# Optimization experiments

Measured on AMD Instinct MI355X. Metric: run time of the kernel, lower is better.

The kernel has to match this reference:

```python
import jax, jax.numpy as jnp
import numpy as np

N = 50000
E = 800000
D_IN, D_HID, D_OUT = 128, 128, 64


def gcn_layer(x, src, dst, W, b, n_nodes):
    # GCNConv: h = W x; add self-loops; symmetric normalization deg^-1/2;
    # scatter-add messages from src to dst; add bias.
    h = x @ W  # [N, d_out]
    loop = jnp.arange(n_nodes, dtype=src.dtype)
    src_sl = jnp.concatenate([src, loop])  # [E+N]
    dst_sl = jnp.concatenate([dst, loop])
    deg = jax.ops.segment_sum(jnp.ones_like(dst_sl, dtype=h.dtype), dst_sl,
                              num_segments=n_nodes)  # in-degree incl. self-loop
    dis = jnp.where(deg > 0, jax.lax.rsqrt(deg), 0.0)
    norm = dis[src_sl] * dis[dst_sl]  # [E+N]
    msg = h[src_sl] * norm[:, None]  # gather + scale
    out = jax.ops.segment_sum(msg, dst_sl, num_segments=n_nodes)
    return out + b


def setup_inputs() -> dict:
    key = jax.random.key(0)
    ks = jax.random.split(key, 8)
    x = jax.random.normal(ks[0], (N, D_IN), dtype=jnp.float32)
    edge_index = jax.random.randint(ks[1], (2, E), 0, N, dtype=jnp.int32)
    def glorot(k, fan_in, fan_out):
        s = jnp.sqrt(6.0 / (fan_in + fan_out))
        return jax.random.uniform(k, (fan_in, fan_out), jnp.float32, -s, s)
    return {
        "x": x,
        "edge_index": edge_index,
        "W1": glorot(ks[2], D_IN, D_HID),  "b1": jnp.zeros((D_HID,), jnp.float32),
        "W2": glorot(ks[3], D_HID, D_HID), "b2": jnp.zeros((D_HID,), jnp.float32),
        "W3": glorot(ks[4], D_HID, D_OUT), "b3": jnp.zeros((D_OUT,), jnp.float32),
    }


def reference(x, edge_index, W1, b1, W2, b2, W3, b3):
    src, dst = edge_index[0], edge_index[1]
    n = x.shape[0]
    h = jax.nn.relu(gcn_layer(x, src, dst, W1, b1, n))
    h = jax.nn.relu(gcn_layer(h, src, dst, W2, b2, n))
    return gcn_layer(h, src, dst, W3, b3, n)
```

## Files before the change

kernel.cpp:

```cpp
#include <hip/hip_runtime.h>
#include <hip/hip_fp16.h>
#include <math.h>


typedef _Float16 half8 __attribute__((ext_vector_type(8)));
typedef float f32x4 __attribute__((ext_vector_type(4)));

__global__ void count_kernel(const int* __restrict__ dst, int* __restrict__ counts,
                             int* __restrict__ rank, int E) {
    int i = blockIdx.x * blockDim.x + threadIdx.x;
    int st = gridDim.x * blockDim.x;
    for (; i < E; i += st) rank[i] = atomicAdd(&counts[dst[i]], 1);
}

__global__ __launch_bounds__(256) void block_sum_kernel(const int* __restrict__ counts,
                                                        int* __restrict__ bsum, int n) {
    const int b = blockIdx.x;
    const int t = threadIdx.x;
    const int idx = b * 256 + t;
    int v = (idx < n) ? counts[idx] : 0;
#pragma unroll
    for (int o = 32; o > 0; o >>= 1) v += __shfl_down(v, o, 64);
    __shared__ int ws[4];
    if ((t & 63) == 0) ws[t >> 6] = v;
    __syncthreads();
    if (t == 0) bsum[b] = ws[0] + ws[1] + ws[2] + ws[3];
}

__global__ __launch_bounds__(256) void small_scan_kernel(int* __restrict__ bsum, int nb) {
    __shared__ int sm[256];
    const int t = threadIdx.x;
    int v = (t < nb) ? bsum[t] : 0;
    sm[t] = v;
    __syncthreads();
    for (int o = 1; o < 256; o <<= 1) {
        int x = (t >= o) ? sm[t - o] : 0;
        __syncthreads();
        sm[t] += x;
        __syncthreads();
    }
    if (t < nb) bsum[t] = sm[t] - v;
}

__global__ __launch_bounds__(256) void scan_block_kernel(const int* __restrict__ counts,
                                                         const int* __restrict__ bsum,
                                                         int* __restrict__ offs,
                                                         float* __restrict__ dis,
                                                         int n, int E) {
    const int b = blockIdx.x;
    const int t = threadIdx.x;
    const int idx = b * 256 + t;
    int v = (idx < n) ? counts[idx] : 0;
    if (idx < n) dis[idx] = rsqrtf((float)(v + 1));
    __shared__ int sm[256];
    sm[t] = v;
    __syncthreads();
    for (int o = 1; o < 256; o <<= 1) {
        int x = (t >= o) ? sm[t - o] : 0;
        __syncthreads();
        sm[t] += x;
        __syncthreads();
    }
    if (idx < n) offs[idx] = bsum[b] + sm[t] - v;
    if (idx == n) offs[n] = E;
}

__global__ void fill_kernel(const int* __restrict__ src, const int* __restrict__ dst,
                            const int* __restrict__ offs, const int* __restrict__ rank,
                            int* __restrict__ csr_s, int E) {
    int i = blockIdx.x * blockDim.x + threadIdx.x;
    int st = gridDim.x * blockDim.x;
    for (; i < E; i += st) {
        int p = offs[dst[i]] + rank[i];
        csr_s[p] = src[i];
    }
}

__global__ __launch_bounds__(256) void wsplit_kernel(const float* __restrict__ W1,
                                                     const float* __restrict__ W2,
                                                     const float* __restrict__ W3,
                                                     _Float16* __restrict__ hi,
                                                     _Float16* __restrict__ lo) {
    int idx = blockIdx.x * 256 + threadIdx.x;
    if (idx >= 40960) return;
    float v;
    if (idx < 16384) {
        int c = idx >> 7, k = idx & 127;
        v = W1[k * 128 + c];
    } else if (idx < 32768) {
        int j = idx - 16384;
        int c = j >> 7, k = j & 127;
        v = W2[k * 128 + c];
    } else {
        int j = idx - 32768;
        int c = j >> 7, k = j & 127;
        v = W3[k * 64 + c];
    }
    _Float16 h = (_Float16)v;
    hi[idx] = h;
    lo[idx] = (_Float16)(v - (float)h);
}

template <int NOUT, bool FROM_F32>
__device__ __forceinline__ void gemm_core(const half8* __restrict__ XhV,
                                          const _Float16* __restrict__ WThi,
                                          const _Float16* __restrict__ WTlo,
                                          const float* __restrict__ dis,
                                          _Float16* __restrict__ Y, int nrows,
                                          const float4* X4) {
    constexpr int CT = NOUT / 16;
    const int wave = threadIdx.x >> 6;
    const int lane = threadIdx.x & 63;
    const int lrow = lane & 15;
    const int lk = lane >> 4;
    const int r0 = (blockIdx.x * 4 + wave) * 32;

    const f32x4 Z = {0.f, 0.f, 0.f, 0.f};
    f32x4 acc[2][CT];
#pragma unroll
    for (int a = 0; a < 2; ++a)
#pragma unroll
        for (int b = 0; b < CT; ++b) acc[a][b] = Z;

    const half8* WhiV = (const half8*)WThi;
    const half8* WloV = (const half8*)WTlo;

    int ar0 = r0 + lrow;
    int ar1 = r0 + 16 + lrow;
    if (ar0 > nrows - 1) ar0 = nrows - 1;
    if (ar1 > nrows - 1) ar1 = nrows - 1;

#pragma unroll
    for (int ks = 0; ks < 4; ++ks) {
        const int kidx = ks * 4 + lk;
        half8 a0h, a1h, a0l, a1l;
        if constexpr (FROM_F32) {
            float4 u0 = X4[(size_t)ar0 * 32 + 2 * kidx];
            float4 u1 = X4[(size_t)ar0 * 32 + 2 * kidx + 1];
            float4 w0 = X4[(size_t)ar1 * 32 + 2 * kidx];
            float4 w1 = X4[(size_t)ar1 * 32 + 2 * kidx + 1];
            float v0[8] = {u0.x, u0.y, u0.z, u0.w, u1.x, u1.y, u1.z, u1.w};
            float v1[8] = {w0.x, w0.y, w0.z, w0.w, w1.x, w1.y, w1.z, w1.w};
#pragma unroll
            for (int j = 0; j < 8; ++j) {
                _Float16 hh = (_Float16)v0[j];
                a0h[j] = hh;
                a0l[j] = (_Float16)(v0[j] - (float)hh);
                _Float16 gg = (_Float16)v1[j];
                a1h[j] = gg;
                a1l[j] = (_Float16)(v1[j] - (float)gg);
            }
        } else {
            a0h = XhV[(size_t)ar0 * 16 + kidx];
            a1h = XhV[(size_t)ar1 * 16 + kidx];
        }
#pragma unroll
        for (int ct = 0; ct < CT; ++ct) {
            const size_t bidx = (size_t)(ct * 16 + lrow) * 16 + kidx;
            half8 bh = WhiV[bidx];
            half8 bl = WloV[bidx];
            if constexpr (FROM_F32) {
                acc[0][ct] = __builtin_amdgcn_mfma_f32_16x16x32_f16(a0l, bh, acc[0][ct], 0, 0, 0);
                acc[1][ct] = __builtin_amdgcn_mfma_f32_16x16x32_f16(a1l, bh, acc[1][ct], 0, 0, 0);
            }
            acc[0][ct] = __builtin_amdgcn_mfma_f32_16x16x32_f16(a0h, bl, acc[0][ct], 0, 0, 0);
            acc[0][ct] = __builtin_amdgcn_mfma_f32_16x16x32_f16(a0h, bh, acc[0][ct], 0, 0, 0);
            acc[1][ct] = __builtin_amdgcn_mfma_f32_16x16x32_f16(a1h, bl, acc[1][ct], 0, 0, 0);
            acc[1][ct] = __builtin_amdgcn_mfma_f32_16x16x32_f16(a1h, bh, acc[1][ct], 0, 0, 0);
        }
    }

    const int orow = r0 + lk * 4;
#pragma unroll
    for (int rt = 0; rt < 2; ++rt) {
#pragma unroll
        for (int r = 0; r < 4; ++r) {
            int row = orow + rt * 16 + r;
            if (row < nrows) {
                float dd = dis[row];
#pragma unroll
                for (int ct = 0; ct < CT; ++ct) {
                    Y[(size_t)row * NOUT + ct * 16 + lrow] =
                        (_Float16)(dd * acc[rt][ct][r]);
                }
            }
        }
    }
}

template <int NOUT>
__global__ __launch_bounds__(256) void gemm_mfma(const _Float16* __restrict__ Xh,
                                                 const _Float16* __restrict__ WThi,
                                                 const _Float16* __restrict__ WTlo,
                                                 const float* __restrict__ dis,
                                                 _Float16* __restrict__ Y, int nrows) {
    gemm_core<NOUT, false>((const half8*)Xh, WThi, WTlo, dis, Y, nrows, nullptr);
}

__global__ __launch_bounds__(256) void gemm_mfma_l1(const float* __restrict__ X,
                                                    const _Float16* __restrict__ WThi,
                                                    const _Float16* __restrict__ WTlo,
                                                    const float* __restrict__ dis,
                                                    _Float16* __restrict__ Y, int nrows) {
    gemm_core<128, true>(nullptr, WThi, WTlo, dis, Y, nrows, (const float4*)X);
}

#define ACC8(_v)                                                                    \
    do {                                                                            \
        float2 _f;                                                                  \
        _f = __half22float2(*reinterpret_cast<const __half2*>(&(_v).x));            \
        a0 += _f.x; a1 += _f.y;                                                     \
        _f = __half22float2(*reinterpret_cast<const __half2*>(&(_v).y));            \
        a2 += _f.x; a3 += _f.y;                                                     \
        _f = __half22float2(*reinterpret_cast<const __half2*>(&(_v).z));            \
        a4 += _f.x; a5 += _f.y;                                                     \
        _f = __half22float2(*reinterpret_cast<const __half2*>(&(_v).w));            \
        a6 += _f.x; a7 += _f.y;                                                     \
    } while (0)

#define ACC8W(_v, _scale)                                                           \
    do {                                                                            \
        float2 _f;                                                                  \
        _f = __half22float2(*reinterpret_cast<const __half2*>(&(_v).x));            \
        a0 = fmaf((_scale), _f.x, a0); a1 = fmaf((_scale), _f.y, a1);               \
        _f = __half22float2(*reinterpret_cast<const __half2*>(&(_v).y));            \
        a2 = fmaf((_scale), _f.x, a2); a3 = fmaf((_scale), _f.y, a3);               \
        _f = __half22float2(*reinterpret_cast<const __half2*>(&(_v).z));            \
        a4 = fmaf((_scale), _f.x, a4); a5 = fmaf((_scale), _f.y, a5);               \
        _f = __half22float2(*reinterpret_cast<const __half2*>(&(_v).w));            \
        a6 = fmaf((_scale), _f.x, a6); a7 = fmaf((_scale), _f.y, a7);               \
    } while (0)

template <bool RELU, bool F16OUT>
__global__ __launch_bounds__(256) void agg128_kernel(const __half* __restrict__ h,
                                                     const float* __restrict__ dis,
                                                     const int* __restrict__ offs,
                                                     const int* __restrict__ csr_s,
                                                     const float* __restrict__ bias,
                                                     float* __restrict__ outf,
                                                     __half* __restrict__ oh16, int n) {
    const int d = blockIdx.x * 4 + (threadIdx.x >> 6);
    if (d >= n) return;
    const int lane = threadIdx.x & 63;
    const int g = lane >> 4;
    const int p = lane & 15;
    const int beg = offs[d];
    const int end = offs[d + 1];
    const uint4* hv = (const uint4*)h;

    float a0 = 0.f, a1 = 0.f, a2 = 0.f, a3 = 0.f;
    float a4 = 0.f, a5 = 0.f, a6 = 0.f, a7 = 0.f;

    int i = beg;
    for (; i + 16 <= end; i += 16) {
        int r0 = csr_s[i + g];
        int r1 = csr_s[i + 4 + g];
        int r2 = csr_s[i + 8 + g];
        int r3 = csr_s[i + 12 + g];
        uint4 v0 = hv[(size_t)r0 * 16 + p];
        uint4 v1 = hv[(size_t)r1 * 16 + p];
        uint4 v2 = hv[(size_t)r2 * 16 + p];
        uint4 v3 = hv[(size_t)r3 * 16 + p];
        ACC8(v0); ACC8(v1); ACC8(v2); ACC8(v3);
    }
    if (i + 8 <= end) {
        int r0 = csr_s[i + g];
        int r1 = csr_s[i + 4 + g];
        uint4 v0 = hv[(size_t)r0 * 16 + p];
        uint4 v1 = hv[(size_t)r1 * 16 + p];
        ACC8(v0); ACC8(v1);
        i += 8;
    }
    if (i + 4 <= end) {
        int r0 = csr_s[i + g];
        uint4 v0 = hv[(size_t)r0 * 16 + p];
        ACC8(v0);
        i += 4;
    }
    {
        int m = end - i;
        int row = (g < m) ? csr_s[i + g] : d;
        float wt = (g <= m) ? 1.f : 0.f;
        uint4 v = hv[(size_t)row * 16 + p];
        ACC8W(v, wt);
    }

    a0 += __shfl_xor(a0, 16); a0 += __shfl_xor(a0, 32);
    a1 += __shfl_xor(a1, 16); a1 += __shfl_xor(a1, 32);
    a2 += __shfl_xor(a2, 16); a2 += __shfl_xor(a2, 32);
    a3 += __shfl_xor(a3, 16); a3 += __shfl_xor(a3, 32);
    a4 += __shfl_xor(a4, 16); a4 += __shfl_xor(a4, 32);
    a5 += __shfl_xor(a5, 16); a5 += __shfl_xor(a5, 32);
    a6 += __shfl_xor(a6, 16); a6 += __shfl_xor(a6, 32);
    a7 += __shfl_xor(a7, 16); a7 += __shfl_xor(a7, 32);

    if (lane < 16) {
        float dd = dis[d];
        float4 b0 = ((const float4*)bias)[2 * p];
        float4 b1 = ((const float4*)bias)[2 * p + 1];
        float r0 = fmaf(dd, a0, b0.x);
        float r1 = fmaf(dd, a1, b0.y);
        float r2 = fmaf(dd, a2, b0.z);
        float r3 = fmaf(dd, a3, b0.w);
        float r4 = fmaf(dd, a4, b1.x);
        float r5 = fmaf(dd, a5, b1.y);
        float r6 = fmaf(dd, a6, b1.z);
        float r7 = fmaf(dd, a7, b1.w);
        if (RELU) {
            r0 = fmaxf(r0, 0.f); r1 = fmaxf(r1, 0.f);
            r2 = fmaxf(r2, 0.f); r3 = fmaxf(r3, 0.f);
            r4 = fmaxf(r4, 0.f); r5 = fmaxf(r5, 0.f);
            r6 = fmaxf(r6, 0.f); r7 = fmaxf(r7, 0.f);
        }
        if constexpr (F16OUT) {
            __half2 q0 = __halves2half2(__float2half(r0), __float2half(r1));
            __half2 q1 = __halves2half2(__float2half(r2), __float2half(r3));
            __half2 q2 = __halves2half2(__float2half(r4), __float2half(r5));
            __half2 q3 = __halves2half2(__float2half(r6), __float2half(r7));
            uint4 uh;
            uh.x = *reinterpret_cast<unsigned*>(&q0);
            uh.y = *reinterpret_cast<unsigned*>(&q1);
            uh.z = *reinterpret_cast<unsigned*>(&q2);
            uh.w = *reinterpret_cast<unsigned*>(&q3);
            ((uint4*)oh16)[(size_t)d * 16 + p] = uh;
        } else {
            ((float4*)outf)[(size_t)d * 32 + 2 * p] = make_float4(r0, r1, r2, r3);
            ((float4*)outf)[(size_t)d * 32 + 2 * p + 1] = make_float4(r4, r5, r6, r7);
        }
    }
}

__global__ __launch_bounds__(256) void agg64_kernel(const __half* __restrict__ h,
                                                    const float* __restrict__ dis,
                                                    const int* __restrict__ offs,
                                                    const int* __restrict__ csr_s,
                                                    const float* __restrict__ bias,
                                                    float* __restrict__ outf, int n) {
    const int d = blockIdx.x * 4 + (threadIdx.x >> 6);
    if (d >= n) return;
    const int lane = threadIdx.x & 63;
    const int g = lane >> 3;
    const int p = lane & 7;
    const int beg = offs[d];
    const int end = offs[d + 1];
    const uint4* hv = (const uint4*)h;

    float a0 = 0.f, a1 = 0.f, a2 = 0.f, a3 = 0.f;
    float a4 = 0.f, a5 = 0.f, a6 = 0.f, a7 = 0.f;

    int i = beg;
    for (; i + 16 <= end; i += 16) {
        int r0 = csr_s[i + g];
        int r1 = csr_s[i + 8 + g];
        uint4 v0 = hv[(size_t)r0 * 8 + p];
        uint4 v1 = hv[(size_t)r1 * 8 + p];
        ACC8(v0); ACC8(v1);
    }
    if (i + 8 <= end) {
        int r0 = csr_s[i + g];
        uint4 v0 = hv[(size_t)r0 * 8 + p];
        ACC8(v0);
        i += 8;
    }
    {
        int m = end - i;
        int row = (g < m) ? csr_s[i + g] : d;
        float wt = (g <= m) ? 1.f : 0.f;
        uint4 v = hv[(size_t)row * 8 + p];
        ACC8W(v, wt);
    }

    a0 += __shfl_xor(a0, 8); a0 += __shfl_xor(a0, 16); a0 += __shfl_xor(a0, 32);
    a1 += __shfl_xor(a1, 8); a1 += __shfl_xor(a1, 16); a1 += __shfl_xor(a1, 32);
    a2 += __shfl_xor(a2, 8); a2 += __shfl_xor(a2, 16); a2 += __shfl_xor(a2, 32);
    a3 += __shfl_xor(a3, 8); a3 += __shfl_xor(a3, 16); a3 += __shfl_xor(a3, 32);
    a4 += __shfl_xor(a4, 8); a4 += __shfl_xor(a4, 16); a4 += __shfl_xor(a4, 32);
    a5 += __shfl_xor(a5, 8); a5 += __shfl_xor(a5, 16); a5 += __shfl_xor(a5, 32);
    a6 += __shfl_xor(a6, 8); a6 += __shfl_xor(a6, 16); a6 += __shfl_xor(a6, 32);
    a7 += __shfl_xor(a7, 8); a7 += __shfl_xor(a7, 16); a7 += __shfl_xor(a7, 32);

    if (lane < 8) {
        float dd = dis[d];
        float4 b0 = ((const float4*)bias)[2 * p];
        float4 b1 = ((const float4*)bias)[2 * p + 1];
        float r0 = fmaf(dd, a0, b0.x);
        float r1 = fmaf(dd, a1, b0.y);
        float r2 = fmaf(dd, a2, b0.z);
        float r3 = fmaf(dd, a3, b0.w);
        float r4 = fmaf(dd, a4, b1.x);
        float r5 = fmaf(dd, a5, b1.y);
        float r6 = fmaf(dd, a6, b1.z);
        float r7 = fmaf(dd, a7, b1.w);
        ((float4*)outf)[(size_t)d * 16 + 2 * p] = make_float4(r0, r1, r2, r3);
        ((float4*)outf)[(size_t)d * 16 + 2 * p + 1] = make_float4(r4, r5, r6, r7);
    }
}


extern "C" void kernel_launch(void* const* d_in, const int* in_sizes, int n_in,
                              void* d_out, int out_size, void* d_ws, size_t ws_size,
                              hipStream_t stream) {
    const float* x  = (const float*)d_in[0];
    const int*   ei = (const int*)d_in[1];
    const float* W1 = (const float*)d_in[2];
    const float* b1 = (const float*)d_in[3];
    const float* W2 = (const float*)d_in[4];
    const float* b2 = (const float*)d_in[5];
    const float* W3 = (const float*)d_in[6];
    const float* b3 = (const float*)d_in[7];

    const int N = in_sizes[0] / 128;
    const int E = in_sizes[1] / 2;
    const int* src = ei;
    const int* dst = ei + E;
    float* out = (float*)d_out;

    char* w = (char*)d_ws;
    auto take = [&](size_t bytes) -> void* {
        void* p = (void*)w;
        w += (bytes + 255) & ~(size_t)255;
        return p;
    };
    int*      counts = (int*)take((size_t)N * 4);
    int*      offs   = (int*)take((size_t)(N + 1) * 4);
    float*    dis    = (float*)take((size_t)N * 4);
    int*      bsum   = (int*)take((size_t)1024 * 4);
    int*      csr_s  = (int*)take((size_t)E * 4);
    _Float16* G16    = (_Float16*)take((size_t)N * 128 * 2);
    _Float16* H16    = (_Float16*)take((size_t)N * 128 * 2);
    _Float16* Whi    = (_Float16*)take((size_t)40960 * 2);
    _Float16* Wlo    = (_Float16*)take((size_t)40960 * 2);
    int*      rank   = (int*)G16;

    const int NBLK = (N + 256) / 256;

    hipMemsetAsync(counts, 0, (size_t)N * 4, stream);
    count_kernel<<<2048, 256, 0, stream>>>(dst, counts, rank, E);
    block_sum_kernel<<<NBLK, 256, 0, stream>>>(counts, bsum, N);
    small_scan_kernel<<<1, 256, 0, stream>>>(bsum, NBLK);
    scan_block_kernel<<<NBLK, 256, 0, stream>>>(counts, bsum, offs, dis, N, E);
    fill_kernel<<<2048, 256, 0, stream>>>(src, dst, offs, rank, csr_s, E);

    wsplit_kernel<<<160, 256, 0, stream>>>(W1, W2, W3, Whi, Wlo);

    const int gblocks = (N + 127) / 128;
    const int ablocks = (N + 3) / 4;

    gemm_mfma_l1<<<gblocks, 256, 0, stream>>>(x, Whi, Wlo, dis, G16, N);
    agg128_kernel<true, true><<<ablocks, 256, 0, stream>>>(
        (const __half*)G16, dis, offs, csr_s, b1, nullptr, (__half*)H16, N);
    gemm_mfma<128><<<gblocks, 256, 0, stream>>>(H16, Whi + 16384, Wlo + 16384,
                                                dis, G16, N);
    agg128_kernel<true, true><<<ablocks, 256, 0, stream>>>(
        (const __half*)G16, dis, offs, csr_s, b2, nullptr, (__half*)H16, N);
    gemm_mfma<64><<<gblocks, 256, 0, stream>>>(H16, Whi + 32768, Wlo + 32768,
                                               dis, G16, N);
    agg64_kernel<<<ablocks, 256, 0, stream>>>((const __half*)G16, dis, offs, csr_s,
                                              b3, out, N);
}
```

Measured before the change: 215.1 us.

## Build CSR with atomic cursors and halve GEMM rows per wave

The CSR build no longer stores a per-edge rank array in the count pass. It copies the offsets into a cursor array and has the fill pass claim slots with atomicAdd, which removes the rank write and read but adds a device memcpy and a second round of atomics. Separately, each GEMM wave now computes 16 rows instead of 32, doubling the block count. This raises parallelism and lowers register use, but loads the weights twice as often per row. Neighbor order inside each CSR row becomes nondeterministic, so the float summation order can vary between runs.

New measurement: 280.2 us. 30.3% more time.

```diff
diff --git a/kernel.cpp b/kernel.cpp
--- a/kernel.cpp
+++ b/kernel.cpp
@@ -6,11 +6,10 @@
 typedef _Float16 half8 __attribute__((ext_vector_type(8)));
 typedef float f32x4 __attribute__((ext_vector_type(4)));
 
-__global__ void count_kernel(const int* __restrict__ dst, int* __restrict__ counts,
-                             int* __restrict__ rank, int E) {
+__global__ void count_kernel(const int* __restrict__ dst, int* __restrict__ counts, int E) {
     int i = blockIdx.x * blockDim.x + threadIdx.x;
     int st = gridDim.x * blockDim.x;
-    for (; i < E; i += st) rank[i] = atomicAdd(&counts[dst[i]], 1);
+    for (; i < E; i += st) atomicAdd(&counts[dst[i]], 1);
 }
 
 __global__ __launch_bounds__(256) void block_sum_kernel(const int* __restrict__ counts,
@@ -66,12 +65,11 @@
 }
 
 __global__ void fill_kernel(const int* __restrict__ src, const int* __restrict__ dst,
-                            const int* __restrict__ offs, const int* __restrict__ rank,
-                            int* __restrict__ csr_s, int E) {
+                            int* __restrict__ cursor, int* __restrict__ csr_s, int E) {
     int i = blockIdx.x * blockDim.x + threadIdx.x;
     int st = gridDim.x * blockDim.x;
     for (; i < E; i += st) {
-        int p = offs[dst[i]] + rank[i];
+        int p = atomicAdd(&cursor[dst[i]], 1);
         csr_s[p] = src[i];
     }
 }
@@ -113,46 +111,35 @@
     const int lane = threadIdx.x & 63;
     const int lrow = lane & 15;
     const int lk = lane >> 4;
-    const int r0 = (blockIdx.x * 4 + wave) * 32;
+    const int r0 = (blockIdx.x * 4 + wave) * 16;
 
     const f32x4 Z = {0.f, 0.f, 0.f, 0.f};
-    f32x4 acc[2][CT];
-#pragma unroll
-    for (int a = 0; a < 2; ++a)
-#pragma unroll
-        for (int b = 0; b < CT; ++b) acc[a][b] = Z;
+    f32x4 acc[CT];
+#pragma unroll
+    for (int b = 0; b < CT; ++b) acc[b] = Z;
 
     const half8* WhiV = (const half8*)WThi;
     const half8* WloV = (const half8*)WTlo;
 
     int ar0 = r0 + lrow;
-    int ar1 = r0 + 16 + lrow;
     if (ar0 > nrows - 1) ar0 = nrows - 1;
-    if (ar1 > nrows - 1) ar1 = nrows - 1;
 
 #pragma unroll
     for (int ks = 0; ks < 4; ++ks) {
         const int kidx = ks * 4 + lk;
-        half8 a0h, a1h, a0l, a1l;
+        half8 a0h, a0l;
         if constexpr (FROM_F32) {
             float4 u0 = X4[(size_t)ar0 * 32 + 2 * kidx];
             float4 u1 = X4[(size_t)ar0 * 32 + 2 * kidx + 1];
-            float4 w0 = X4[(size_t)ar1 * 32 + 2 * kidx];
-            float4 w1 = X4[(size_t)ar1 * 32 + 2 * kidx + 1];
             float v0[8] = {u0.x, u0.y, u0.z, u0.w, u1.x, u1.y, u1.z, u1.w};
-            float v1[8] = {w0.x, w0.y, w0.z, w0.w, w1.x, w1.y, w1.z, w1.w};
 #pragma unroll
             for (int j = 0; j < 8; ++j) {
                 _Float16 hh = (_Float16)v0[j];
                 a0h[j] = hh;
                 a0l[j] = (_Float16)(v0[j] - (float)hh);
-                _Float16 gg = (_Float16)v1[j];
-                a1h[j] = gg;
-                a1l[j] = (_Float16)(v1[j] - (float)gg);
             }
         } else {
             a0h = XhV[(size_t)ar0 * 16 + kidx];
-            a1h = XhV[(size_t)ar1 * 16 + kidx];
         }
 #pragma unroll
         for (int ct = 0; ct < CT; ++ct) {
@@ -160,29 +147,22 @@
             half8 bh = WhiV[bidx];
             half8 bl = WloV[bidx];
             if constexpr (FROM_F32) {
-                acc[0][ct] = __builtin_amdgcn_mfma_f32_16x16x32_f16(a0l, bh, acc[0][ct], 0, 0, 0);
-                acc[1][ct] = __builtin_amdgcn_mfma_f32_16x16x32_f16(a1l, bh, acc[1][ct], 0, 0, 0);
+                acc[ct] = __builtin_amdgcn_mfma_f32_16x16x32_f16(a0l, bh, acc[ct], 0, 0, 0);
             }
-            acc[0][ct] = __builtin_amdgcn_mfma_f32_16x16x32_f16(a0h, bl, acc[0][ct], 0, 0, 0);
-            acc[0][ct] = __builtin_amdgcn_mfma_f32_16x16x32_f16(a0h, bh, acc[0][ct], 0, 0, 0);
-            acc[1][ct] = __builtin_amdgcn_mfma_f32_16x16x32_f16(a1h, bl, acc[1][ct], 0, 0, 0);
-            acc[1][ct] = __builtin_amdgcn_mfma_f32_16x16x32_f16(a1h, bh, acc[1][ct], 0, 0, 0);
+            acc[ct] = __builtin_amdgcn_mfma_f32_16x16x32_f16(a0h, bl, acc[ct], 0, 0, 0);
+            acc[ct] = __builtin_amdgcn_mfma_f32_16x16x32_f16(a0h, bh, acc[ct], 0, 0, 0);
         }
     }
 
     const int orow = r0 + lk * 4;
 #pragma unroll
-    for (int rt = 0; rt < 2; ++rt) {
-#pragma unroll
-        for (int r = 0; r < 4; ++r) {
-            int row = orow + rt * 16 + r;
-            if (row < nrows) {
-                float dd = dis[row];
-#pragma unroll
-                for (int ct = 0; ct < CT; ++ct) {
-                    Y[(size_t)row * NOUT + ct * 16 + lrow] =
-                        (_Float16)(dd * acc[rt][ct][r]);
-                }
+    for (int r = 0; r < 4; ++r) {
+        int row = orow + r;
+        if (row < nrows) {
+            float dd = dis[row];
+#pragma unroll
+            for (int ct = 0; ct < CT; ++ct) {
+                Y[(size_t)row * NOUT + ct * 16 + lrow] = (_Float16)(dd * acc[ct][r]);
             }
         }
     }
@@ -423,6 +403,7 @@
     };
     int*      counts = (int*)take((size_t)N * 4);
     int*      offs   = (int*)take((size_t)(N + 1) * 4);
+    int*      cursor = (int*)take((size_t)N * 4);
     float*    dis    = (float*)take((size_t)N * 4);
     int*      bsum   = (int*)take((size_t)1024 * 4);
     int*      csr_s  = (int*)take((size_t)E * 4);
@@ -430,20 +411,20 @@
     _Float16* H16    = (_Float16*)take((size_t)N * 128 * 2);
     _Float16* Whi    = (_Float16*)take((size_t)40960 * 2);
     _Float16* Wlo    = (_Float16*)take((size_t)40960 * 2);
-    int*      rank   = (int*)G16;
 
     const int NBLK = (N + 256) / 256;
 
     hipMemsetAsync(counts, 0, (size_t)N * 4, stream);
-    count_kernel<<<2048, 256, 0, stream>>>(dst, counts, rank, E);
+    count_kernel<<<2048, 256, 0, stream>>>(dst, counts, E);
     block_sum_kernel<<<NBLK, 256, 0, stream>>>(counts, bsum, N);
     small_scan_kernel<<<1, 256, 0, stream>>>(bsum, NBLK);
     scan_block_kernel<<<NBLK, 256, 0, stream>>>(counts, bsum, offs, dis, N, E);
-    fill_kernel<<<2048, 256, 0, stream>>>(src, dst, offs, rank, csr_s, E);
+    hipMemcpyAsync(cursor, offs, (size_t)N * 4, hipMemcpyDeviceToDevice, stream);
+    fill_kernel<<<2048, 256, 0, stream>>>(src, dst, cursor, csr_s, E);
 
     wsplit_kernel<<<160, 256, 0, stream>>>(W1, W2, W3, Whi, Wlo);
 
-    const int gblocks = (N + 127) / 128;
+    const int gblocks = (N + 63) / 64;
     const int ablocks = (N + 3) / 4;
 
     gemm_mfma_l1<<<gblocks, 256, 0, stream>>>(x, Whi, Wlo, dis, G16, N);
```
